# Kernel tuning notes

Hardware: AMD Instinct MI355X
Metric: run time of the kernel (lower is better)

The kernel has to match this reference:

```python
import jax, jax.numpy as jnp
import numpy as np

B, N, C, T, H, G = 8, 256, 128, 64, 4, 12
D = C // H
EPS = 1e-6


def _linear_params(key, din, dout):
    k1, k2 = jax.random.split(key)
    lim = 1.0 / np.sqrt(din)
    W = jax.random.uniform(k1, (din, dout), jnp.float32, -lim, lim)
    b = jax.random.uniform(k2, (dout,), jnp.float32, -lim, lim)
    return W, b


def setup_inputs():
    key = jax.random.key(0)
    ks = jax.random.split(key, 12)
    inp = {
        'feat': jax.random.normal(ks[0], (B, N, C), jnp.float32),
        'centers': jax.random.normal(ks[1], (B, N, 3), jnp.float32),
        'corners': jax.random.normal(ks[2], (B, N, 8, 3), jnp.float32),
        'lang_tokens': jax.random.normal(ks[3], (B, T, C), jnp.float32),
    }
    names = ['q', 'k', 'v', 'o', 'rel', 'tk', 'tv', 'bias']
    dims = [(C, C), (C, C), (C, C), (C, C), (G, C), (C, C), (C, C), (C, H)]
    for nm, (di, do), kk in zip(names, dims, ks[4:]):
        W, b = _linear_params(kk, di, do)
        inp[f'W{nm}'] = W
        inp[f'b{nm}'] = b
    return inp


def _build_geom(centers, corners):
    # centers: (B,N,3), corners: (B,N,8,3) -> (B,N,N,12)
    rel_vec = centers[:, None, :, :] - centers[:, :, None, :]  # [b,i,j] = c_j - c_i
    dist = jnp.linalg.norm(rel_vec, axis=-1, keepdims=True)
    horiz = jnp.linalg.norm(rel_vec[..., :2], axis=-1, keepdims=True)
    dz = rel_vec[..., 2:3]
    cos_elev = dz / (dist + EPS)
    dist_log = jnp.log(dist + EPS)
    sizes = corners.max(axis=2) - corners.min(axis=2)  # (B,N,3)
    size_i = sizes[:, :, None, :]
    size_j = sizes[:, None, :, :]
    size_diff = size_j - size_i
    size_ratio = size_j / (size_i + EPS)
    return jnp.concatenate([rel_vec, dist_log, horiz, cos_elev, size_diff, size_ratio], axis=-1)


def reference(feat, centers, corners, lang_tokens,
              Wq, bq, Wk, bk, Wv, bv, Wo, bo,
              Wrel, brel, Wtk, btk, Wtv, btv, Wbias, bbias):
    geom = _build_geom(centers, corners)              # (B,N,N,G)
    rel_feat = geom.reshape(B, N * N, G) @ Wrel + brel  # (B,NN,C)
    k_txt = lang_tokens @ Wtk + btk                   # (B,T,C)
    v_txt = lang_tokens @ Wtv + btv
    scores = jnp.einsum('brc,btc->brt', rel_feat, k_txt) / np.sqrt(C).astype(np.float32)
    alpha = jax.nn.softmax(scores, axis=-1)
    ctx = jnp.einsum('brt,btc->brc', alpha, v_txt)
    bias_flat = (rel_feat + ctx) @ Wbias + bbias      # (B,NN,H)
    bias = bias_flat.reshape(B, N, N, H).transpose(0, 3, 1, 2)  # (B,H,N,N)
    q = (feat @ Wq + bq).reshape(B, N, H, D).transpose(0, 2, 1, 3)
    k = (feat @ Wk + bk).reshape(B, N, H, D).transpose(0, 2, 1, 3)
    v = (feat @ Wv + bv).reshape(B, N, H, D).transpose(0, 2, 1, 3)
    logits = jnp.einsum('bhnd,bhmd->bhnm', q, k) / np.sqrt(D).astype(np.float32) + bias
    attn = jax.nn.softmax(logits, axis=-1)
    out = jnp.einsum('bhnm,bhmd->bhnd', attn, v)
    out = out.transpose(0, 2, 1, 3).reshape(B, N, C)
    return out @ Wo + bo
```

## Files before the change

### kernel.cpp

```cpp
#include <hip/hip_runtime.h>
#include <math.h>

namespace {
constexpr int kB = 8, kN = 256, kC = 128, kT = 64, kH = 4, kG = 12, kD = 32;
constexpr float kEps = 1e-6f;
constexpr float kInvSqrtC = 0.08838834764831845f;
constexpr float kInvSqrtD = 0.17677669529663687f;

constexpr int WS_Q     = 0;
constexpr int WS_KT    = WS_Q + kB*kN*kC;
constexpr int WS_V     = WS_KT + kB*kN*kC;
constexpr int WS_SIZES = WS_V + kB*kN*kC;
constexpr int WS_KTXT  = WS_SIZES + kB*kN*3;
constexpr int WS_VTXT  = WS_KTXT + kB*kT*kC;
constexpr int WS_WKF   = WS_VTXT + kB*kT*kC;
constexpr int WS_SK    = WS_WKF + kB*kG*kT;
constexpr int WS_VB    = WS_SK + kB*kT;
constexpr int WS_WB1   = WS_VB + kB*kT*kH;
constexpr int WS_CB    = WS_WB1 + kG*kH;
constexpr int WS_BIAS  = WS_CB + kH;

constexpr int kProjQKV  = (kB*kN)/4;
constexpr int kProjTxt  = (kB*kT)/4;
constexpr int kProjSize = (kB*kN)/256;

constexpr int kTasksPerB = kG*kT + kT + kT*kH;
constexpr int kTasksAll  = kB*kTasksPerB;
constexpr int kTasksTot  = kTasksAll + kG*kH + kH;
constexpr int kFoldBlocks = (kTasksTot + 3) / 4;

constexpr int TI = 2;
}

static __global__ __launch_bounds__(256)
void proj_kernel(const float* __restrict__ feat, const float* __restrict__ lang,
                 const float* __restrict__ corners,
                 const float* __restrict__ Wq, const float* __restrict__ bq,
                 const float* __restrict__ Wk, const float* __restrict__ bk,
                 const float* __restrict__ Wv, const float* __restrict__ bv,
                 const float* __restrict__ Wtk, const float* __restrict__ btk,
                 const float* __restrict__ Wtv, const float* __restrict__ btv,
                 float* __restrict__ ws)
{
  const int blk = blockIdx.x;
  const int tid = threadIdx.x;
  __shared__ float rows[4][kC];

  if (blk < kProjQKV) {
    const int r0 = blk * 4;
    rows[tid >> 7][tid & 127] = feat[(size_t)r0*kC + tid];
    rows[(tid + 256) >> 7][tid & 127] = feat[(size_t)r0*kC + tid + 256];
    __syncthreads();

    const int c = tid & 127;
    const int p = tid >> 7;
    const int ra = p*2, rb = p*2 + 1;

    float aq0 = bq[c], aq1 = aq0;
    float ak0 = bk[c], ak1 = ak0;
    float av0 = bv[c], av1 = av0;
#pragma unroll 4
    for (int d = 0; d < kC; ++d) {
      const float wq = Wq[d*kC + c], wk = Wk[d*kC + c], wv = Wv[d*kC + c];
      const float fa = rows[ra][d], fb = rows[rb][d];
      aq0 = fmaf(fa, wq, aq0); aq1 = fmaf(fb, wq, aq1);
      ak0 = fmaf(fa, wk, ak0); ak1 = fmaf(fb, wk, ak1);
      av0 = fmaf(fa, wv, av0); av1 = fmaf(fb, wv, av1);
    }

    const int gra = r0 + ra, grb = r0 + rb;
    const int bb = r0 / kN, n0 = r0 % kN;
    ws[WS_Q + (size_t)gra*kC + c] = aq0 * kInvSqrtD;
    ws[WS_Q + (size_t)grb*kC + c] = aq1 * kInvSqrtD;
    ws[WS_KT + (size_t)bb*kC*kN + c*kN + n0 + ra] = ak0;
    ws[WS_KT + (size_t)bb*kC*kN + c*kN + n0 + rb] = ak1;
    ws[WS_V + (size_t)gra*kC + c] = av0;
    ws[WS_V + (size_t)grb*kC + c] = av1;
  } else if (blk < kProjQKV + kProjTxt) {
    const int r0 = (blk - kProjQKV) * 4;
    rows[tid >> 7][tid & 127] = lang[(size_t)r0*kC + tid];
    rows[(tid + 256) >> 7][tid & 127] = lang[(size_t)r0*kC + tid + 256];
    __syncthreads();

    const int c = tid & 127;
    const int p = tid >> 7;
    const int ra = p*2, rb = p*2 + 1;

    float ak0 = btk[c], ak1 = ak0;
    float av0 = btv[c], av1 = av0;
#pragma unroll 4
    for (int d = 0; d < kC; ++d) {
      const float wk = Wtk[d*kC + c], wv = Wtv[d*kC + c];
      const float fa = rows[ra][d], fb = rows[rb][d];
      ak0 = fmaf(fa, wk, ak0); ak1 = fmaf(fb, wk, ak1);
      av0 = fmaf(fa, wv, av0); av1 = fmaf(fb, wv, av1);
    }
    ws[WS_KTXT + (size_t)(r0 + ra)*kC + c] = ak0;
    ws[WS_KTXT + (size_t)(r0 + rb)*kC + c] = ak1;
    ws[WS_VTXT + (size_t)(r0 + ra)*kC + c] = av0;
    ws[WS_VTXT + (size_t)(r0 + rb)*kC + c] = av1;
  } else {
    const int n = (blk - kProjQKV - kProjTxt) * 256 + tid;
    const float* cp = corners + (size_t)n * 24;
    float mn0 = cp[0], mn1 = cp[1], mn2 = cp[2];
    float mx0 = mn0, mx1 = mn1, mx2 = mn2;
#pragma unroll
    for (int k = 1; k < 8; ++k) {
      const float v0 = cp[k*3+0], v1 = cp[k*3+1], v2 = cp[k*3+2];
      mn0 = fminf(mn0, v0); mx0 = fmaxf(mx0, v0);
      mn1 = fminf(mn1, v1); mx1 = fmaxf(mx1, v1);
      mn2 = fminf(mn2, v2); mx2 = fmaxf(mx2, v2);
    }
    ws[WS_SIZES + n*3 + 0] = mx0 - mn0;
    ws[WS_SIZES + n*3 + 1] = mx1 - mn1;
    ws[WS_SIZES + n*3 + 2] = mx2 - mn2;
  }
}

static __global__ __launch_bounds__(256)
void fold_kernel(const float* __restrict__ Wrel, const float* __restrict__ brel,
                 const float* __restrict__ Wbias, const float* __restrict__ bbias,
                 float* __restrict__ ws)
{
  const int task = blockIdx.x * 4 + (threadIdx.x >> 6);
  const int lane = threadIdx.x & 63;
  if (task >= kTasksTot) return;

  const float* x; const float* y; float* outp; float addend = 0.f;
  float mul = 1.f;
  int ystride4 = 0;

  if (task < kTasksAll) {
    const int b = task / kTasksPerB;
    const int tt = task % kTasksPerB;
    const float* ktxt = ws + WS_KTXT + (size_t)b*kT*kC;
    const float* vtxt = ws + WS_VTXT + (size_t)b*kT*kC;
    if (tt < kG*kT) {
      const int g = tt >> 6, t = tt & 63;
      x = Wrel + g*kC; y = ktxt + t*kC; mul = kInvSqrtC;
      outp = ws + WS_WKF + b*kG*kT + g*kT + t;
    } else if (tt < kG*kT + kT) {
      const int t = tt - kG*kT;
      x = brel; y = ktxt + t*kC; mul = kInvSqrtC;
      outp = ws + WS_SK + b*kT + t;
    } else {
      const int idx = tt - kG*kT - kT;
      const int t = idx >> 2, h = idx & 3;
      x = vtxt + t*kC; y = Wbias + h; ystride4 = 1;
      outp = ws + WS_VB + b*kT*kH + t*kH + h;
    }
  } else {
    const int tt = task - kTasksAll;
    if (tt < kG*kH) {
      const int g = tt >> 2, h = tt & 3;
      x = Wrel + g*kC; y = Wbias + h; ystride4 = 1;
      outp = ws + WS_WB1 + g*kH + h;
    } else {
      const int h = tt - kG*kH;
      x = brel; y = Wbias + h; ystride4 = 1;
      addend = bbias[h];
      outp = ws + WS_CB + h;
    }
  }

  float p;
  if (ystride4) {
    p = x[lane]*y[lane*kH] + x[lane+64]*y[(lane+64)*kH];
  } else {
    p = x[lane]*y[lane] + x[lane+64]*y[lane+64];
  }
#pragma unroll
  for (int off = 32; off >= 1; off >>= 1) p += __shfl_xor(p, off, 64);
  if (lane == 0) *outp = p * mul + addend;
}

static __global__ __launch_bounds__(256, 4)
void bias_kernel(const float* __restrict__ centers,
                 const float* __restrict__ ws_ro, float* __restrict__ ws)
{
  const int i = blockIdx.x;
  const int b = blockIdx.y;
  const int j = threadIdx.x;

  const float* cI = centers + (size_t)(b*kN + i)*3;
  const float* sI = ws_ro + WS_SIZES + (size_t)(b*kN + i)*3;
  const float cix = cI[0], ciy = cI[1], ciz = cI[2];
  const float six = sI[0], siy = sI[1], siz = sI[2];

  const float* cJ = centers + (size_t)(b*kN + j)*3;
  const float* sJ = ws_ro + WS_SIZES + (size_t)(b*kN + j)*3;

  float g[kG];
  {
    const float dx = cJ[0] - cix;
    const float dy = cJ[1] - ciy;
    const float dz = cJ[2] - ciz;
    const float dist = sqrtf(dx*dx + dy*dy + dz*dz);
    const float horiz = sqrtf(dx*dx + dy*dy);
    g[0] = dx; g[1] = dy; g[2] = dz;
    g[3] = __logf(dist + kEps);
    g[4] = horiz;
    g[5] = dz / (dist + kEps);
    const float sjx = sJ[0], sjy = sJ[1], sjz = sJ[2];
    g[6] = sjx - six; g[7] = sjy - siy; g[8] = sjz - siz;
    g[9]  = sjx / (six + kEps);
    g[10] = sjy / (siy + kEps);
    g[11] = sjz / (siz + kEps);
  }

  const float4* __restrict__ wkf4 = (const float4*)(ws_ro + WS_WKF + b*kG*kT);
  const float4* __restrict__ sk4  = (const float4*)(ws_ro + WS_SK  + b*kT);
  const float4* __restrict__ vb4  = (const float4*)(ws_ro + WS_VB  + b*kT*kH);
  const float* __restrict__ wb1 = ws_ro + WS_WB1;
  const float* __restrict__ cbv = ws_ro + WS_CB;

  float m = -1e30f, ssum = 0.f;
  float a0 = 0.f, a1 = 0.f, a2 = 0.f, a3 = 0.f;
#pragma unroll
  for (int ch = 0; ch < 2; ++ch) {
    float4 sc4[8];
#pragma unroll
    for (int t4 = 0; t4 < 8; ++t4) sc4[t4] = sk4[ch*8 + t4];
#pragma unroll
    for (int gg = 0; gg < kG; ++gg) {
      const float gv = g[gg];
#pragma unroll
      for (int t4 = 0; t4 < 8; ++t4) {
        const float4 wv = wkf4[gg*(kT/4) + ch*8 + t4];
        sc4[t4].x = fmaf(gv, wv.x, sc4[t4].x);
        sc4[t4].y = fmaf(gv, wv.y, sc4[t4].y);
        sc4[t4].z = fmaf(gv, wv.z, sc4[t4].z);
        sc4[t4].w = fmaf(gv, wv.w, sc4[t4].w);
      }
    }
    float cm = -1e30f;
#pragma unroll
    for (int t4 = 0; t4 < 8; ++t4)
      cm = fmaxf(cm, fmaxf(fmaxf(sc4[t4].x, sc4[t4].y), fmaxf(sc4[t4].z, sc4[t4].w)));
    const float nm = fmaxf(m, cm);
    const float scale = __expf(m - nm);
    ssum *= scale; a0 *= scale; a1 *= scale; a2 *= scale; a3 *= scale;
#pragma unroll
    for (int t4 = 0; t4 < 8; ++t4) {
      const int t = ch*32 + t4*4;
      const float e0 = __expf(sc4[t4].x - nm);
      const float e1 = __expf(sc4[t4].y - nm);
      const float e2 = __expf(sc4[t4].z - nm);
      const float e3 = __expf(sc4[t4].w - nm);
      ssum += e0 + e1 + e2 + e3;
      const float4 v0 = vb4[t+0], v1 = vb4[t+1], v2 = vb4[t+2], v3 = vb4[t+3];
      a0 = fmaf(e0, v0.x, a0); a1 = fmaf(e0, v0.y, a1);
      a2 = fmaf(e0, v0.z, a2); a3 = fmaf(e0, v0.w, a3);
      a0 = fmaf(e1, v1.x, a0); a1 = fmaf(e1, v1.y, a1);
      a2 = fmaf(e1, v1.z, a2); a3 = fmaf(e1, v1.w, a3);
      a0 = fmaf(e2, v2.x, a0); a1 = fmaf(e2, v2.y, a1);
      a2 = fmaf(e2, v2.z, a2); a3 = fmaf(e2, v2.w, a3);
      a0 = fmaf(e3, v3.x, a0); a1 = fmaf(e3, v3.y, a1);
      a2 = fmaf(e3, v3.z, a2); a3 = fmaf(e3, v3.w, a3);
    }
    m = nm;
  }
  const float invSsum = 1.f / ssum;

  float4 bias;
  bias.x = a0*invSsum + cbv[0];
  bias.y = a1*invSsum + cbv[1];
  bias.z = a2*invSsum + cbv[2];
  bias.w = a3*invSsum + cbv[3];
#pragma unroll
  for (int gg = 0; gg < kG; ++gg) {
    const float gv = g[gg];
    bias.x = fmaf(gv, wb1[gg*kH + 0], bias.x);
    bias.y = fmaf(gv, wb1[gg*kH + 1], bias.y);
    bias.z = fmaf(gv, wb1[gg*kH + 2], bias.z);
    bias.w = fmaf(gv, wb1[gg*kH + 3], bias.w);
  }

  *(float4*)(ws + WS_BIAS + (size_t)((b*kN + i)*kN + j)*kH) = bias;
}

static __global__ __launch_bounds__(256, 4)
void attn_kernel(const float* __restrict__ Wo, const float* __restrict__ bo,
                 const float* __restrict__ ws, float* __restrict__ out)
{
  const int i0 = blockIdx.x * TI;
  const int b  = blockIdx.y;
  const int tid = threadIdx.x;
  const int j = tid;

  __shared__ float4 s_w4[TI][kN];
  __shared__ float  s_red[4][TI][kH];
  __shared__ float  s_part[8][TI][kC];
  __shared__ float  s_ao[TI][kC];

  const float* __restrict__ kt = ws + WS_KT + (size_t)b*kC*kN;
  const float* __restrict__ qb = ws + WS_Q + (size_t)(b*kN + i0)*kC;

  float acc[TI][kH];
#pragma unroll
  for (int i = 0; i < TI; ++i)
#pragma unroll
    for (int h = 0; h < kH; ++h) acc[i][h] = 0.f;

#pragma unroll
  for (int h = 0; h < kH; ++h) {
#pragma unroll 4
    for (int dd = 0; dd < kD; ++dd) {
      const int d = h*kD + dd;
      const float kv = kt[d*kN + j];
#pragma unroll
      for (int i = 0; i < TI; ++i)
        acc[i][h] = fmaf(qb[i*kC + d], kv, acc[i][h]);
    }
  }

  float lg[TI][kH];
#pragma unroll
  for (int i = 0; i < TI; ++i) {
    const float4 bv = *(const float4*)(ws + WS_BIAS + (size_t)((b*kN + i0 + i)*kN + j)*kH);
    lg[i][0] = acc[i][0] + bv.x;
    lg[i][1] = acc[i][1] + bv.y;
    lg[i][2] = acc[i][2] + bv.z;
    lg[i][3] = acc[i][3] + bv.w;
  }

  const int wave = tid >> 6, lane = tid & 63;
  float mh[TI][kH];
#pragma unroll
  for (int i = 0; i < TI; ++i)
#pragma unroll
    for (int h = 0; h < kH; ++h) {
      float v = lg[i][h];
#pragma unroll
      for (int off = 32; off >= 1; off >>= 1) v = fmaxf(v, __shfl_xor(v, off, 64));
      if (lane == 0) s_red[wave][i][h] = v;
    }
  __syncthreads();
#pragma unroll
  for (int i = 0; i < TI; ++i)
#pragma unroll
    for (int h = 0; h < kH; ++h)
      mh[i][h] = fmaxf(fmaxf(s_red[0][i][h], s_red[1][i][h]),
                       fmaxf(s_red[2][i][h], s_red[3][i][h]));
  __syncthreads();

  float eh[TI][kH];
#pragma unroll
  for (int i = 0; i < TI; ++i)
#pragma unroll
    for (int h = 0; h < kH; ++h) {
      eh[i][h] = __expf(lg[i][h] - mh[i][h]);
      float v = eh[i][h];
#pragma unroll
      for (int off = 32; off >= 1; off >>= 1) v += __shfl_xor(v, off, 64);
      if (lane == 0) s_red[wave][i][h] = v;
    }
  __syncthreads();
#pragma unroll
  for (int i = 0; i < TI; ++i) {
    float4 w;
    float S0 = s_red[0][i][0] + s_red[1][i][0] + s_red[2][i][0] + s_red[3][i][0];
    float S1 = s_red[0][i][1] + s_red[1][i][1] + s_red[2][i][1] + s_red[3][i][1];
    float S2 = s_red[0][i][2] + s_red[1][i][2] + s_red[2][i][2] + s_red[3][i][2];
    float S3 = s_red[0][i][3] + s_red[1][i][3] + s_red[2][i][3] + s_red[3][i][3];
    w.x = eh[i][0] / S0; w.y = eh[i][1] / S1;
    w.z = eh[i][2] / S2; w.w = eh[i][3] / S3;
    s_w4[i][j] = w;
  }
  __syncthreads();

  {
    const int c4  = tid & 31;
    const int grp = tid >> 5;
    const int hh  = c4 >> 3;
    const float4* __restrict__ v4 = (const float4*)(ws + WS_V + (size_t)(b*kN)*kC);
    float4 a4[TI];
#pragma unroll
    for (int i = 0; i < TI; ++i) a4[i] = make_float4(0.f, 0.f, 0.f, 0.f);
#pragma unroll 4
    for (int jj = 0; jj < 32; ++jj) {
      const int jr = grp*32 + jj;
      const float4 vv = v4[jr*(kC/4) + c4];
#pragma unroll
      for (int i = 0; i < TI; ++i) {
        const float w = ((const float*)&s_w4[i][jr])[hh];
        a4[i].x = fmaf(w, vv.x, a4[i].x);
        a4[i].y = fmaf(w, vv.y, a4[i].y);
        a4[i].z = fmaf(w, vv.z, a4[i].z);
        a4[i].w = fmaf(w, vv.w, a4[i].w);
      }
    }
#pragma unroll
    for (int i = 0; i < TI; ++i) *(float4*)&s_part[grp][i][c4*4] = a4[i];
  }
  __syncthreads();
  {
    const int ii = tid >> 7, c = tid & (kC-1);
    float v = 0.f;
#pragma unroll
    for (int gp = 0; gp < 8; ++gp) v += s_part[gp][ii][c];
    s_ao[ii][c] = v;
  }
  __syncthreads();

  {
    const int col = tid & (kC - 1);
    const int seg = tid >> 7;
    float accO[TI];
#pragma unroll
    for (int i = 0; i < TI; ++i) accO[i] = (seg == 0) ? bo[col] : 0.f;
    const int d0 = seg * (kC/2);
#pragma unroll 4
    for (int d = d0; d < d0 + kC/2; ++d) {
      const float w = Wo[d*kC + col];
#pragma unroll
      for (int i = 0; i < TI; ++i) accO[i] = fmaf(s_ao[i][d], w, accO[i]);
    }
#pragma unroll
    for (int i = 0; i < TI; ++i) s_part[seg][i][col] = accO[i];
  }
  __syncthreads();
  {
    const int ii = tid >> 7, c = tid & (kC-1);
    out[(size_t)(b*kN + i0 + ii)*kC + c] = s_part[0][ii][c] + s_part[1][ii][c];
  }
}

extern "C" void kernel_launch(void* const* d_in, const int* in_sizes, int n_in,
                              void* d_out, int out_size, void* d_ws, size_t ws_size,
                              hipStream_t stream)
{
  (void)in_sizes; (void)n_in; (void)out_size; (void)ws_size;
  const float* feat    = (const float*)d_in[0];
  const float* centers = (const float*)d_in[1];
  const float* corners = (const float*)d_in[2];
  const float* lang    = (const float*)d_in[3];
  const float* Wq   = (const float*)d_in[4];
  const float* bq   = (const float*)d_in[5];
  const float* Wk   = (const float*)d_in[6];
  const float* bk   = (const float*)d_in[7];
  const float* Wv   = (const float*)d_in[8];
  const float* bv   = (const float*)d_in[9];
  const float* Wo   = (const float*)d_in[10];
  const float* bo   = (const float*)d_in[11];
  const float* Wrel = (const float*)d_in[12];
  const float* brel = (const float*)d_in[13];
  const float* Wtk  = (const float*)d_in[14];
  const float* btk  = (const float*)d_in[15];
  const float* Wtv  = (const float*)d_in[16];
  const float* btv  = (const float*)d_in[17];
  const float* Wbias = (const float*)d_in[18];
  const float* bbias = (const float*)d_in[19];

  float* ws  = (float*)d_ws;
  float* out = (float*)d_out;

  proj_kernel<<<dim3(kProjQKV + kProjTxt + kProjSize), dim3(256), 0, stream>>>(
      feat, lang, corners, Wq, bq, Wk, bk, Wv, bv, Wtk, btk, Wtv, btv, ws);
  fold_kernel<<<dim3(kFoldBlocks), dim3(256), 0, stream>>>(
      Wrel, brel, Wbias, bbias, ws);
  bias_kernel<<<dim3(kN, kB), dim3(256), 0, stream>>>(centers, ws, ws);
  attn_kernel<<<dim3(kN/TI, kB), dim3(256), 0, stream>>>(Wo, bo, ws, out);
}
```

Measured before the change: 164.8 us.

## Fuse geometric bias computation into attention kernel

Removes the separate bias kernel and computes each (i,j) relative-position bias inside the attention kernel, with each thread handling TI rows for its column j. This drops the write and re-read of the B*N*N*H bias buffer and one kernel launch. In exchange the attention kernel carries the per-pair text-softmax work, which raises register pressure and may lower occupancy.

```diff
diff --git a/kernel.cpp b/kernel.cpp
--- a/kernel.cpp
+++ b/kernel.cpp
@@ -18,7 +18,6 @@
 constexpr int WS_VB    = WS_SK + kB*kT;
 constexpr int WS_WB1   = WS_VB + kB*kT*kH;
 constexpr int WS_CB    = WS_WB1 + kG*kH;
-constexpr int WS_BIAS  = WS_CB + kH;
 
 constexpr int kProjQKV  = (kB*kN)/4;
 constexpr int kProjTxt  = (kB*kT)/4;
@@ -175,113 +174,9 @@
 }
 
 static __global__ __launch_bounds__(256, 4)
-void bias_kernel(const float* __restrict__ centers,
-                 const float* __restrict__ ws_ro, float* __restrict__ ws)
-{
-  const int i = blockIdx.x;
-  const int b = blockIdx.y;
-  const int j = threadIdx.x;
-
-  const float* cI = centers + (size_t)(b*kN + i)*3;
-  const float* sI = ws_ro + WS_SIZES + (size_t)(b*kN + i)*3;
-  const float cix = cI[0], ciy = cI[1], ciz = cI[2];
-  const float six = sI[0], siy = sI[1], siz = sI[2];
-
-  const float* cJ = centers + (size_t)(b*kN + j)*3;
-  const float* sJ = ws_ro + WS_SIZES + (size_t)(b*kN + j)*3;
-
-  float g[kG];
-  {
-    const float dx = cJ[0] - cix;
-    const float dy = cJ[1] - ciy;
-    const float dz = cJ[2] - ciz;
-    const float dist = sqrtf(dx*dx + dy*dy + dz*dz);
-    const float horiz = sqrtf(dx*dx + dy*dy);
-    g[0] = dx; g[1] = dy; g[2] = dz;
-    g[3] = __logf(dist + kEps);
-    g[4] = horiz;
-    g[5] = dz / (dist + kEps);
-    const float sjx = sJ[0], sjy = sJ[1], sjz = sJ[2];
-    g[6] = sjx - six; g[7] = sjy - siy; g[8] = sjz - siz;
-    g[9]  = sjx / (six + kEps);
-    g[10] = sjy / (siy + kEps);
-    g[11] = sjz / (siz + kEps);
-  }
-
-  const float4* __restrict__ wkf4 = (const float4*)(ws_ro + WS_WKF + b*kG*kT);
-  const float4* __restrict__ sk4  = (const float4*)(ws_ro + WS_SK  + b*kT);
-  const float4* __restrict__ vb4  = (const float4*)(ws_ro + WS_VB  + b*kT*kH);
-  const float* __restrict__ wb1 = ws_ro + WS_WB1;
-  const float* __restrict__ cbv = ws_ro + WS_CB;
-
-  float m = -1e30f, ssum = 0.f;
-  float a0 = 0.f, a1 = 0.f, a2 = 0.f, a3 = 0.f;
-#pragma unroll
-  for (int ch = 0; ch < 2; ++ch) {
-    float4 sc4[8];
-#pragma unroll
-    for (int t4 = 0; t4 < 8; ++t4) sc4[t4] = sk4[ch*8 + t4];
-#pragma unroll
-    for (int gg = 0; gg < kG; ++gg) {
-      const float gv = g[gg];
-#pragma unroll
-      for (int t4 = 0; t4 < 8; ++t4) {
-        const float4 wv = wkf4[gg*(kT/4) + ch*8 + t4];
-        sc4[t4].x = fmaf(gv, wv.x, sc4[t4].x);
-        sc4[t4].y = fmaf(gv, wv.y, sc4[t4].y);
-        sc4[t4].z = fmaf(gv, wv.z, sc4[t4].z);
-        sc4[t4].w = fmaf(gv, wv.w, sc4[t4].w);
-      }
-    }
-    float cm = -1e30f;
-#pragma unroll
-    for (int t4 = 0; t4 < 8; ++t4)
-      cm = fmaxf(cm, fmaxf(fmaxf(sc4[t4].x, sc4[t4].y), fmaxf(sc4[t4].z, sc4[t4].w)));
-    const float nm = fmaxf(m, cm);
-    const float scale = __expf(m - nm);
-    ssum *= scale; a0 *= scale; a1 *= scale; a2 *= scale; a3 *= scale;
-#pragma unroll
-    for (int t4 = 0; t4 < 8; ++t4) {
-      const int t = ch*32 + t4*4;
-      const float e0 = __expf(sc4[t4].x - nm);
-      const float e1 = __expf(sc4[t4].y - nm);
-      const float e2 = __expf(sc4[t4].z - nm);
-      const float e3 = __expf(sc4[t4].w - nm);
-      ssum += e0 + e1 + e2 + e3;
-      const float4 v0 = vb4[t+0], v1 = vb4[t+1], v2 = vb4[t+2], v3 = vb4[t+3];
-      a0 = fmaf(e0, v0.x, a0); a1 = fmaf(e0, v0.y, a1);
-      a2 = fmaf(e0, v0.z, a2); a3 = fmaf(e0, v0.w, a3);
-      a0 = fmaf(e1, v1.x, a0); a1 = fmaf(e1, v1.y, a1);
-      a2 = fmaf(e1, v1.z, a2); a3 = fmaf(e1, v1.w, a3);
-      a0 = fmaf(e2, v2.x, a0); a1 = fmaf(e2, v2.y, a1);
-      a2 = fmaf(e2, v2.z, a2); a3 = fmaf(e2, v2.w, a3);
-      a0 = fmaf(e3, v3.x, a0); a1 = fmaf(e3, v3.y, a1);
-      a2 = fmaf(e3, v3.z, a2); a3 = fmaf(e3, v3.w, a3);
-    }
-    m = nm;
-  }
-  const float invSsum = 1.f / ssum;
-
-  float4 bias;
-  bias.x = a0*invSsum + cbv[0];
-  bias.y = a1*invSsum + cbv[1];
-  bias.z = a2*invSsum + cbv[2];
-  bias.w = a3*invSsum + cbv[3];
-#pragma unroll
-  for (int gg = 0; gg < kG; ++gg) {
-    const float gv = g[gg];
-    bias.x = fmaf(gv, wb1[gg*kH + 0], bias.x);
-    bias.y = fmaf(gv, wb1[gg*kH + 1], bias.y);
-    bias.z = fmaf(gv, wb1[gg*kH + 2], bias.z);
-    bias.w = fmaf(gv, wb1[gg*kH + 3], bias.w);
-  }
-
-  *(float4*)(ws + WS_BIAS + (size_t)((b*kN + i)*kN + j)*kH) = bias;
-}
-
-static __global__ __launch_bounds__(256, 4)
-void attn_kernel(const float* __restrict__ Wo, const float* __restrict__ bo,
-                 const float* __restrict__ ws, float* __restrict__ out)
+void fused_attn_kernel(const float* __restrict__ centers,
+                       const float* __restrict__ Wo, const float* __restrict__ bo,
+                       const float* __restrict__ ws, float* __restrict__ out)
 {
   const int i0 = blockIdx.x * TI;
   const int b  = blockIdx.y;
@@ -293,6 +188,106 @@
   __shared__ float  s_part[8][TI][kC];
   __shared__ float  s_ao[TI][kC];
 
+  const float* cJ = centers + (size_t)(b*kN + j)*3;
+  const float* sJ = ws + WS_SIZES + (size_t)(b*kN + j)*3;
+  const float cjx = cJ[0], cjy = cJ[1], cjz = cJ[2];
+  const float sjx = sJ[0], sjy = sJ[1], sjz = sJ[2];
+
+  const float4* __restrict__ wkf4 = (const float4*)(ws + WS_WKF + b*kG*kT);
+  const float4* __restrict__ sk4  = (const float4*)(ws + WS_SK  + b*kT);
+  const float4* __restrict__ vb4  = (const float4*)(ws + WS_VB  + b*kT*kH);
+  const float* __restrict__ wb1 = ws + WS_WB1;
+  const float* __restrict__ cbv = ws + WS_CB;
+
+  float4 bias4[TI];
+#pragma unroll
+  for (int ii = 0; ii < TI; ++ii) {
+    const int i = i0 + ii;
+    const float* cI = centers + (size_t)(b*kN + i)*3;
+    const float* sI = ws + WS_SIZES + (size_t)(b*kN + i)*3;
+
+    float g[kG];
+    {
+      const float dx = cjx - cI[0];
+      const float dy = cjy - cI[1];
+      const float dz = cjz - cI[2];
+      const float dist = sqrtf(dx*dx + dy*dy + dz*dz);
+      const float horiz = sqrtf(dx*dx + dy*dy);
+      g[0] = dx; g[1] = dy; g[2] = dz;
+      g[3] = __logf(dist + kEps);
+      g[4] = horiz;
+      g[5] = dz / (dist + kEps);
+      const float six = sI[0], siy = sI[1], siz = sI[2];
+      g[6] = sjx - six; g[7] = sjy - siy; g[8] = sjz - siz;
+      g[9]  = sjx / (six + kEps);
+      g[10] = sjy / (siy + kEps);
+      g[11] = sjz / (siz + kEps);
+    }
+
+    float m = -1e30f, ssum = 0.f;
+    float a0 = 0.f, a1 = 0.f, a2 = 0.f, a3 = 0.f;
+#pragma unroll
+    for (int ch = 0; ch < 2; ++ch) {
+      float4 sc4[8];
+#pragma unroll
+      for (int t4 = 0; t4 < 8; ++t4) sc4[t4] = sk4[ch*8 + t4];
+#pragma unroll
+      for (int gg = 0; gg < kG; ++gg) {
+        const float gv = g[gg];
+#pragma unroll
+        for (int t4 = 0; t4 < 8; ++t4) {
+          const float4 wv = wkf4[gg*(kT/4) + ch*8 + t4];
+          sc4[t4].x = fmaf(gv, wv.x, sc4[t4].x);
+          sc4[t4].y = fmaf(gv, wv.y, sc4[t4].y);
+          sc4[t4].z = fmaf(gv, wv.z, sc4[t4].z);
+          sc4[t4].w = fmaf(gv, wv.w, sc4[t4].w);
+        }
+      }
+      float cm = -1e30f;
+#pragma unroll
+      for (int t4 = 0; t4 < 8; ++t4)
+        cm = fmaxf(cm, fmaxf(fmaxf(sc4[t4].x, sc4[t4].y), fmaxf(sc4[t4].z, sc4[t4].w)));
+      const float nm = fmaxf(m, cm);
+      const float scale = __expf(m - nm);
+      ssum *= scale; a0 *= scale; a1 *= scale; a2 *= scale; a3 *= scale;
+#pragma unroll
+      for (int t4 = 0; t4 < 8; ++t4) {
+        const int t = ch*32 + t4*4;
+        const float e0 = __expf(sc4[t4].x - nm);
+        const float e1 = __expf(sc4[t4].y - nm);
+        const float e2 = __expf(sc4[t4].z - nm);
+        const float e3 = __expf(sc4[t4].w - nm);
+        ssum += e0 + e1 + e2 + e3;
+        const float4 v0 = vb4[t+0], v1 = vb4[t+1], v2 = vb4[t+2], v3 = vb4[t+3];
+        a0 = fmaf(e0, v0.x, a0); a1 = fmaf(e0, v0.y, a1);
+        a2 = fmaf(e0, v0.z, a2); a3 = fmaf(e0, v0.w, a3);
+        a0 = fmaf(e1, v1.x, a0); a1 = fmaf(e1, v1.y, a1);
+        a2 = fmaf(e1, v1.z, a2); a3 = fmaf(e1, v1.w, a3);
+        a0 = fmaf(e2, v2.x, a0); a1 = fmaf(e2, v2.y, a1);
+        a2 = fmaf(e2, v2.z, a2); a3 = fmaf(e2, v2.w, a3);
+        a0 = fmaf(e3, v3.x, a0); a1 = fmaf(e3, v3.y, a1);
+        a2 = fmaf(e3, v3.z, a2); a3 = fmaf(e3, v3.w, a3);
+      }
+      m = nm;
+    }
+    const float invSsum = 1.f / ssum;
+
+    float4 bias;
+    bias.x = a0*invSsum + cbv[0];
+    bias.y = a1*invSsum + cbv[1];
+    bias.z = a2*invSsum + cbv[2];
+    bias.w = a3*invSsum + cbv[3];
+#pragma unroll
+    for (int gg = 0; gg < kG; ++gg) {
+      const float gv = g[gg];
+      bias.x = fmaf(gv, wb1[gg*kH + 0], bias.x);
+      bias.y = fmaf(gv, wb1[gg*kH + 1], bias.y);
+      bias.z = fmaf(gv, wb1[gg*kH + 2], bias.z);
+      bias.w = fmaf(gv, wb1[gg*kH + 3], bias.w);
+    }
+    bias4[ii] = bias;
+  }
+
   const float* __restrict__ kt = ws + WS_KT + (size_t)b*kC*kN;
   const float* __restrict__ qb = ws + WS_Q + (size_t)(b*kN + i0)*kC;
 
@@ -317,11 +312,10 @@
   float lg[TI][kH];
 #pragma unroll
   for (int i = 0; i < TI; ++i) {
-    const float4 bv = *(const float4*)(ws + WS_BIAS + (size_t)((b*kN + i0 + i)*kN + j)*kH);
-    lg[i][0] = acc[i][0] + bv.x;
-    lg[i][1] = acc[i][1] + bv.y;
-    lg[i][2] = acc[i][2] + bv.z;
-    lg[i][3] = acc[i][3] + bv.w;
+    lg[i][0] = acc[i][0] + bias4[i].x;
+    lg[i][1] = acc[i][1] + bias4[i].y;
+    lg[i][2] = acc[i][2] + bias4[i].z;
+    lg[i][3] = acc[i][3] + bias4[i].w;
   }
 
   const int wave = tid >> 6, lane = tid & 63;
@@ -459,6 +453,6 @@
       feat, lang, corners, Wq, bq, Wk, bk, Wv, bv, Wtk, btk, Wtv, btv, ws);
   fold_kernel<<<dim3(kFoldBlocks), dim3(256), 0, stream>>>(
       Wrel, brel, Wbias, bbias, ws);
-  bias_kernel<<<dim3(kN, kB), dim3(256), 0, stream>>>(centers, ws, ws);
-  attn_kernel<<<dim3(kN/TI, kB), dim3(256), 0, stream>>>(Wo, bo, ws, out);
+  fused_attn_kernel<<<dim3(kN/TI, kB), dim3(256), 0, stream>>>(
+      centers, Wo, bo, ws, out);
 }
```

After: 208.6 us. 26.5% more time.
